# Optimization experiments

Measured on AMD Instinct MI355X. Metric: run time of the kernel, lower is better.

## Reference

```python
import jax, jax.numpy as jnp
import numpy as np

N_NODES = 500_000
N_EDGES = 2_000_000
N_GRAPHS = 20_000
N_PAIRS = 50_000
IN_CH = 64
EMB_CH = 64
HID_CH = 256
OUT_CH = 1


def setup_inputs() -> dict:
    key = jax.random.key(0)
    ks = jax.random.split(key, 10)
    x = jax.random.normal(ks[0], (N_NODES, IN_CH), dtype=jnp.float32)
    edge_index = jax.random.randint(ks[1], (2, N_EDGES), 0, N_NODES, dtype=jnp.int64)
    batch_idx = jnp.sort(jax.random.randint(ks[2], (N_NODES,), 0, N_GRAPHS, dtype=jnp.int64))
    drug_pairs = jax.random.randint(ks[3], (2, N_PAIRS), 0, N_GRAPHS, dtype=jnp.int64)
    s1 = 1.0 / np.sqrt(IN_CH)
    s2 = 1.0 / np.sqrt(EMB_CH)
    s3 = 1.0 / np.sqrt(2 * EMB_CH)
    s4 = 1.0 / np.sqrt(HID_CH)
    return {
        "x": x,
        "edge_index": edge_index,
        "batch_idx": batch_idx,
        "drug_pairs": drug_pairs,
        "W1": jax.random.normal(ks[4], (IN_CH, EMB_CH), jnp.float32) * s1,
        "b1": jnp.zeros((EMB_CH,), jnp.float32),
        "W2": jax.random.normal(ks[5], (EMB_CH, EMB_CH), jnp.float32) * s2,
        "b2": jnp.zeros((EMB_CH,), jnp.float32),
        "Wr1": jax.random.normal(ks[6], (2 * EMB_CH, HID_CH), jnp.float32) * s3,
        "br1": jnp.zeros((HID_CH,), jnp.float32),
        "Wr2": jax.random.normal(ks[7], (HID_CH, OUT_CH), jnp.float32) * s4,
        "br2": jnp.zeros((OUT_CH,), jnp.float32),
    }


def _gcn_conv(x, W, b, src, dst, num_nodes):
    # Standard GCNConv: x' = D^{-1/2} (A + I) D^{-1/2} (x W) + b,
    # with D the degree including self-loops.
    h = x @ W  # [N, C_out]
    ones = jnp.ones((src.shape[0],), h.dtype)
    deg = jax.ops.segment_sum(ones, dst, num_segments=num_nodes) + 1.0  # self-loop
    inv_sqrt = jax.lax.rsqrt(deg)
    norm = inv_sqrt[src] * inv_sqrt[dst]  # [E]
    msg = h[src] * norm[:, None]  # gather + scale, [E, C_out]
    agg = jax.ops.segment_sum(msg, dst, num_segments=num_nodes)
    agg = agg + h * (1.0 / deg)[:, None]  # self-loop term (norm = deg^{-1})
    return agg + b


def reference(x, edge_index, batch_idx, drug_pairs, W1, b1, W2, b2, Wr1, br1, Wr2, br2):
    n = x.shape[0]
    src, dst = edge_index[0], edge_index[1]
    # conv1 -> relu -> dropout(eval: identity)
    h = jax.nn.relu(_gcn_conv(x, W1, b1, src, dst, n))
    # conv2 -> relu -> dropout(eval: identity)
    h = jax.nn.relu(_gcn_conv(h, W2, b2, src, dst, n))
    # scatter_mean pooling: node embeds -> per-graph mean
    sums = jax.ops.segment_sum(h, batch_idx, num_segments=N_GRAPHS)
    counts = jax.ops.segment_sum(jnp.ones((n,), h.dtype), batch_idx, num_segments=N_GRAPHS)
    graph_embeds = sums / jnp.maximum(counts, 1.0)[:, None]  # [G, C]
    # gather drug pair embeddings and concat
    pair_feat = jnp.concatenate(
        [graph_embeds[drug_pairs[0]], graph_embeds[drug_pairs[1]]], axis=-1
    )  # [P, 2C]
    hid = jax.nn.relu(pair_feat @ Wr1 + br1)
    return hid @ Wr2 + br2  # [P, out_channels]
```

## Files before the change

### kernel.cpp

```cpp
#include <hip/hip_runtime.h>
#include <cstdint>

#define N_GRAPHS 20000
#define SCAN_CHUNK 2048
#define NBLK 512
#define SRC_BITS 19

typedef _Float16 half_t;
typedef __attribute__((ext_vector_type(4))) _Float16 half4;
typedef __attribute__((ext_vector_type(8))) _Float16 half8;
typedef __attribute__((ext_vector_type(4))) float f32x4;

__global__ __launch_bounds__(256) void scan1(const int* __restrict__ in, int* __restrict__ out,
                                             int* __restrict__ bsum, int M) {
  __shared__ int lds[256];
  int t = threadIdx.x;
  int base = blockIdx.x * SCAN_CHUNK + t * 8;
  int v[8];
  int s = 0;
#pragma unroll
  for (int i = 0; i < 8; ++i) {
    v[i] = (base + i < M) ? in[base + i] : 0;
    s += v[i];
  }
  lds[t] = s;
  __syncthreads();
  for (int off = 1; off < 256; off <<= 1) {
    int x = (t >= off) ? lds[t - off] : 0;
    __syncthreads();
    lds[t] += x;
    __syncthreads();
  }
  if (t == 255) bsum[blockIdx.x] = lds[255];
  int run = (t > 0) ? lds[t - 1] : 0;
#pragma unroll
  for (int i = 0; i < 8; ++i) {
    if (base + i <= M) out[base + i] = run;
    run += v[i];
  }
}

__global__ __launch_bounds__(256) void scan2(int* __restrict__ bsum, int nb) {
  __shared__ int lds[256];
  int t = threadIdx.x;
  lds[t] = (t < nb) ? bsum[t] : 0;
  __syncthreads();
  for (int off = 1; off < 256; off <<= 1) {
    int x = (t >= off) ? lds[t - off] : 0;
    __syncthreads();
    lds[t] += x;
    __syncthreads();
  }
  if (t < nb) bsum[t] = (t > 0) ? lds[t - 1] : 0;
}

__global__ void scan3(int* __restrict__ out, const int* __restrict__ bsum, int Mp1) {
  int i = blockIdx.x * blockDim.x + threadIdx.x;
  if (i < Mp1) out[i] += bsum[i / SCAN_CHUNK];
}

__global__ __launch_bounds__(256) void bucket_hist(const int* __restrict__ dst,
                                                   int* __restrict__ bcnt, int E, int nbuck) {
  __shared__ int h[512];
  for (int i = threadIdx.x; i < 512; i += 256) h[i] = 0;
  __syncthreads();
  int per = (E + NBLK - 1) / NBLK;
  int s = blockIdx.x * per;
  int e = min(s + per, E);
  for (int i = s + threadIdx.x; i < e; i += 256) atomicAdd(&h[dst[i] >> 10], 1);
  __syncthreads();
  for (int b = threadIdx.x; b < nbuck; b += 256) bcnt[(long)b * NBLK + blockIdx.x] = h[b];
}

__global__ __launch_bounds__(256) void bucket_scatter(const int* __restrict__ src,
                                                      const int* __restrict__ dst,
                                                      const int* __restrict__ bbase,
                                                      int* __restrict__ sed, int E, int nbuck) {
  __shared__ int h[512];
  for (int b = threadIdx.x; b < nbuck; b += 256) h[b] = bbase[(long)b * NBLK + blockIdx.x];
  __syncthreads();
  int per = (E + NBLK - 1) / NBLK;
  int s = blockIdx.x * per;
  int e = min(s + per, E);
  for (int i = s + threadIdx.x; i < e; i += 256) {
    int d = dst[i];
    int pos = atomicAdd(&h[d >> 10], 1);
    sed[pos] = ((d & 1023) << SRC_BITS) | src[i];
  }
}

__global__ __launch_bounds__(256) void node_csr(const int* __restrict__ sed,
                                                const int* __restrict__ bbase,
                                                int2* __restrict__ rsp, float* __restrict__ isq,
                                                int* __restrict__ csr, int E, int nbuck, int N,
                                                int PARK) {
  __shared__ int h[1024];
  __shared__ int ws[256];
  __shared__ int cur[1024];
  int b = blockIdx.x;
  int n0 = b << 10;
  int nn = min(1024, N - n0);
  int t = threadIdx.x;
  for (int i = t; i < 1024; i += 256) h[i] = 0;
  __syncthreads();
  int s = bbase[(long)b * NBLK];
  int e = (b + 1 < nbuck) ? bbase[(long)(b + 1) * NBLK] : E;
  for (int i = s + t; i < e; i += 256) atomicAdd(&h[((unsigned)sed[i]) >> SRC_BITS], 1);
  __syncthreads();
  int v0 = h[4 * t], v1 = h[4 * t + 1], v2 = h[4 * t + 2], v3 = h[4 * t + 3];
  int p0 = (v0 + 3) & ~3, p1 = (v1 + 3) & ~3, p2 = (v2 + 3) & ~3, p3 = (v3 + 3) & ~3;
  ws[t] = p0 + p1 + p2 + p3;
  __syncthreads();
  for (int off = 1; off < 256; off <<= 1) {
    int x = (t >= off) ? ws[t - off] : 0;
    __syncthreads();
    ws[t] += x;
    __syncthreads();
  }
  int pbase = s + 3072 * b;
  int st0 = pbase + ((t > 0) ? ws[t - 1] : 0);
  int st1 = st0 + p0, st2 = st1 + p1, st3 = st2 + p2;
  int i0 = 4 * t;
  cur[i0] = st0;
  cur[i0 + 1] = st1;
  cur[i0 + 2] = st2;
  cur[i0 + 3] = st3;
  if (i0 < nn) { rsp[n0 + i0] = make_int2(st0, st0 + p0); isq[n0 + i0] = rsqrtf((float)(v0 + 1)); }
  if (i0 + 1 < nn) { rsp[n0 + i0 + 1] = make_int2(st1, st1 + p1); isq[n0 + i0 + 1] = rsqrtf((float)(v1 + 1)); }
  if (i0 + 2 < nn) { rsp[n0 + i0 + 2] = make_int2(st2, st2 + p2); isq[n0 + i0 + 2] = rsqrtf((float)(v2 + 1)); }
  if (i0 + 3 < nn) { rsp[n0 + i0 + 3] = make_int2(st3, st3 + p3); isq[n0 + i0 + 3] = rsqrtf((float)(v3 + 1)); }
  __syncthreads();
  for (int i = s + t; i < e; i += 256) {
    int v = sed[i];
    int pos = atomicAdd(&cur[((unsigned)v) >> SRC_BITS], 1);
    csr[pos] = v & ((1 << SRC_BITS) - 1);
  }
  __syncthreads();
  for (int j = v0; j < p0; ++j) csr[st0 + j] = N;
  for (int j = v1; j < p1; ++j) csr[st1 + j] = N;
  for (int j = v2; j < p2; ++j) csr[st2 + j] = N;
  for (int j = v3; j < p3; ++j) csr[st3 + j] = N;
  if (b == 0 && t < 64) csr[PARK + t] = N;
}

__global__ __launch_bounds__(256) void scale_cast(const float* __restrict__ x,
                                                  const float* __restrict__ isq,
                                                  half_t* __restrict__ xs1,
                                                  half_t* __restrict__ xs2,
                                                  long nocts, int N) {
  long i = (long)blockIdx.x * 256 + threadIdx.x;
  if (blockIdx.x == 0 && threadIdx.x < 16) {
    const half8 z = {(half_t)0, (half_t)0, (half_t)0, (half_t)0,
                     (half_t)0, (half_t)0, (half_t)0, (half_t)0};
    half_t* base = (threadIdx.x < 8) ? xs1 : xs2;
    ((half8*)(base + (size_t)N * 64))[threadIdx.x & 7] = z;
  }
  if (i >= nocts) return;
  int node = (int)(i >> 3);
  float s = isq[node];
  float4 vlo = ((const float4*)x)[i * 2];
  float4 vhi = ((const float4*)x)[i * 2 + 1];
  half8 h;
  h[0] = (half_t)(vlo.x * s);
  h[1] = (half_t)(vlo.y * s);
  h[2] = (half_t)(vlo.z * s);
  h[3] = (half_t)(vlo.w * s);
  h[4] = (half_t)(vhi.x * s);
  h[5] = (half_t)(vhi.y * s);
  h[6] = (half_t)(vhi.z * s);
  h[7] = (half_t)(vhi.w * s);
  ((half8*)xs1)[i] = h;
}

__global__ __launch_bounds__(256) void gather_fused(const half_t* __restrict__ xs,
                                                    const int* __restrict__ csr,
                                                    const int2* __restrict__ rsp,
                                                    const float* __restrict__ isq,
                                                    const float* __restrict__ W,
                                                    const float* __restrict__ bias,
                                                    half_t* __restrict__ out, int N,
                                                    int PARK, int scale_out) {
  __shared__ half_t Wt[64][72];
  __shared__ half_t exh[32][72];
  __shared__ float idv[32];
  int tid = threadIdx.x;
  {
    int c = tid & 63;
    int kb = (tid >> 6) * 16;
#pragma unroll
    for (int i = 0; i < 16; ++i) Wt[c][kb + i] = (half_t)W[(kb + i) * 64 + c];
  }

  int lane = tid & 63;
  int sub = lane & 7;
  int grp = lane >> 3;
  int li = tid >> 3;
  int wid = (blockIdx.x * blockDim.x + tid) >> 6;
  long d0 = (long)wid * 8;
  int d = (int)d0 + grp;
  bool vd = (d0 < N) && (d < N);
  int dd = vd ? d : N - 1;
  int2 rr = rsp[dd];
  int jj = vd ? rr.x : PARK;
  int je = vd ? rr.y : PARK;
  float id = isq[dd];
  const uint8_t* xb = (const uint8_t*)xs;
  uint32_t co = (uint32_t)sub << 4;
  float ac[8];
  {
    half8 sv = *(const half8*)(xb + (((uint32_t)dd << 7) + co));
#pragma unroll
    for (int c = 0; c < 8; ++c) ac[c] = (float)sv[c];
  }
  jj = (jj < je) ? jj : PARK;
  while (__any(jj != PARK)) {
    int s0 = csr[jj];
    int s1 = csr[jj + 1];
    int s2 = csr[jj + 2];
    int s3 = csr[jj + 3];
    half8 v0 = *(const half8*)(xb + (((uint32_t)s0 << 7) + co));
    half8 v1 = *(const half8*)(xb + (((uint32_t)s1 << 7) + co));
    half8 v2 = *(const half8*)(xb + (((uint32_t)s2 << 7) + co));
    half8 v3 = *(const half8*)(xb + (((uint32_t)s3 << 7) + co));
    half8 sum = (v0 + v1) + (v2 + v3);
#pragma unroll
    for (int c = 0; c < 8; ++c) ac[c] += (float)sum[c];
    jj += 4;
    jj = (jj < je) ? jj : PARK;
  }
  {
    half8 ah;
#pragma unroll
    for (int c = 0; c < 8; ++c) ah[c] = (half_t)ac[c];
    *(half8*)&exh[li][sub * 8] = ah;
    if (sub == 0) idv[li] = id;
  }
  __syncthreads();

  int w = tid >> 6;
  int lr = lane & 15;
  int lk = lane >> 4;
  long d0b = (long)blockIdx.x * 32;
#pragma unroll
  for (int t2 = 0; t2 < 2; ++t2) {
    int tile = w * 2 + t2;
    int mt = tile >> 2;
    int nt = tile & 3;
    f32x4 acc = {0.f, 0.f, 0.f, 0.f};
#pragma unroll
    for (int ks = 0; ks < 2; ++ks) {
      half8 a = *(const half8*)&exh[mt * 16 + lr][ks * 32 + lk * 8];
      half8 b = *(const half8*)&Wt[nt * 16 + lr][ks * 32 + lk * 8];
      acc = __builtin_amdgcn_mfma_f32_16x16x32_f16(a, b, acc, 0, 0, 0);
    }
    float bv = bias[nt * 16 + lr];
#pragma unroll
    for (int j = 0; j < 4; ++j) {
      int nl = mt * 16 + lk * 4 + j;
      long dn = d0b + nl;
      if (dn < N) {
        float id2 = idv[nl];
        float m = scale_out ? id2 : 1.f;
        float r = fmaxf(fmaf(acc[j], id2, bv), 0.f) * m;
        out[dn * 64 + nt * 16 + lr] = (half_t)r;
      }
    }
  }
}

__global__ void seg_offsets(const int* __restrict__ batch, int* __restrict__ off, int N, int G) {
  int i = blockIdx.x * blockDim.x + threadIdx.x;
  if (i >= N) return;
  int b = batch[i];
  if (i == 0) {
    for (int g = 0; g <= b; ++g) off[g] = 0;
  } else {
    int pb = batch[i - 1];
    for (int g = pb + 1; g <= b; ++g) off[g] = i;
  }
  if (i == N - 1) {
    for (int g = b + 1; g <= G; ++g) off[g] = N;
  }
}

__global__ void pool_mean(const half_t* __restrict__ e2, const int* __restrict__ off,
                          float* __restrict__ ge, int G) {
  int lane = threadIdx.x & 63;
  int wid = (blockIdx.x * blockDim.x + threadIdx.x) >> 6;
  int nw = (gridDim.x * blockDim.x) >> 6;
  int c8 = lane & 7;
  int rp = lane >> 3;
  for (int g = wid; g < G; g += nw) {
    int s = off[g];
    int e = off[g + 1];
    float acc[8];
#pragma unroll
    for (int c = 0; c < 8; ++c) acc[c] = 0.f;
    for (int n = s + rp; n < e; n += 8) {
      half8 v = *(const half8*)&e2[(long)n * 64 + c8 * 8];
#pragma unroll
      for (int c = 0; c < 8; ++c) acc[c] += (float)v[c];
    }
#pragma unroll
    for (int c = 0; c < 8; ++c) {
      acc[c] += __shfl_xor(acc[c], 8, 64);
      acc[c] += __shfl_xor(acc[c], 16, 64);
      acc[c] += __shfl_xor(acc[c], 32, 64);
    }
    if (rp == 0) {
      float inv = 1.f / fmaxf((float)(e - s), 1.f);
      float4 lo = make_float4(acc[0] * inv, acc[1] * inv, acc[2] * inv, acc[3] * inv);
      float4 hi = make_float4(acc[4] * inv, acc[5] * inv, acc[6] * inv, acc[7] * inv);
      *(float4*)&ge[(long)g * 64 + c8 * 8] = lo;
      *(float4*)&ge[(long)g * 64 + c8 * 8 + 4] = hi;
    }
  }
}

#define PPB 64
__global__ __launch_bounds__(256) void pair_mlp(const float* __restrict__ ge,
                                                const int* __restrict__ dp,
                                                const float* __restrict__ Wr1,
                                                const float* __restrict__ br1,
                                                const float* __restrict__ Wr2,
                                                const float* __restrict__ br2,
                                                float* __restrict__ out, int P) {
  __shared__ float feat[PPB][128];
  __shared__ int pidx[2][PPB];
  int tid = threadIdx.x;
  int base = blockIdx.x * PPB;
  if (tid < PPB) {
    int p = base + tid;
    pidx[0][tid] = (p < P) ? dp[p] : 0;
    pidx[1][tid] = (p < P) ? dp[P + p] : 0;
  }
  __syncthreads();
#pragma unroll
  for (int i = 0; i < 8; ++i) {
    int u = tid + i * 256;
    int p = u >> 5;
    int k = (u & 31) * 4;
    int g = (k < 64) ? pidx[0][p] : pidx[1][p];
    *(float4*)&feat[p][k] = *(const float4*)&ge[(long)g * 64 + (k & 63)];
  }
  __syncthreads();
  int jg = tid & 63;
  int j0 = jg * 4;
  int pg = tid >> 6;
  int pb = pg * 16;
  float acc[16][4];
#pragma unroll
  for (int p = 0; p < 16; ++p)
#pragma unroll
    for (int j = 0; j < 4; ++j) acc[p][j] = 0.f;
  for (int k4 = 0; k4 < 32; ++k4) {
    float4 w0 = *(const float4*)&Wr1[(k4 * 4 + 0) * 256 + j0];
    float4 w1 = *(const float4*)&Wr1[(k4 * 4 + 1) * 256 + j0];
    float4 w2 = *(const float4*)&Wr1[(k4 * 4 + 2) * 256 + j0];
    float4 w3 = *(const float4*)&Wr1[(k4 * 4 + 3) * 256 + j0];
#pragma unroll
    for (int p = 0; p < 16; ++p) {
      float4 f = *(const float4*)&feat[pb + p][k4 * 4];
      acc[p][0] = fmaf(f.x, w0.x, acc[p][0]);
      acc[p][1] = fmaf(f.x, w0.y, acc[p][1]);
      acc[p][2] = fmaf(f.x, w0.z, acc[p][2]);
      acc[p][3] = fmaf(f.x, w0.w, acc[p][3]);
      acc[p][0] = fmaf(f.y, w1.x, acc[p][0]);
      acc[p][1] = fmaf(f.y, w1.y, acc[p][1]);
      acc[p][2] = fmaf(f.y, w1.z, acc[p][2]);
      acc[p][3] = fmaf(f.y, w1.w, acc[p][3]);
      acc[p][0] = fmaf(f.z, w2.x, acc[p][0]);
      acc[p][1] = fmaf(f.z, w2.y, acc[p][1]);
      acc[p][2] = fmaf(f.z, w2.z, acc[p][2]);
      acc[p][3] = fmaf(f.z, w2.w, acc[p][3]);
      acc[p][0] = fmaf(f.w, w3.x, acc[p][0]);
      acc[p][1] = fmaf(f.w, w3.y, acc[p][1]);
      acc[p][2] = fmaf(f.w, w3.z, acc[p][2]);
      acc[p][3] = fmaf(f.w, w3.w, acc[p][3]);
    }
  }
  float4 b1v = *(const float4*)&br1[j0];
  float4 w2v = *(const float4*)&Wr2[j0];
  float br2v = br2[0];
#pragma unroll
  for (int p = 0; p < 16; ++p) {
    float v = fmaxf(acc[p][0] + b1v.x, 0.f) * w2v.x;
    v = fmaf(fmaxf(acc[p][1] + b1v.y, 0.f), w2v.y, v);
    v = fmaf(fmaxf(acc[p][2] + b1v.z, 0.f), w2v.z, v);
    v = fmaf(fmaxf(acc[p][3] + b1v.w, 0.f), w2v.w, v);
    for (int o = 32; o > 0; o >>= 1) v += __shfl_down(v, o, 64);
    if (jg == 0) {
      int pp = base + pb + p;
      if (pp < P) out[pp] = v + br2v;
    }
  }
}

extern "C" void kernel_launch(void* const* d_in, const int* in_sizes, int n_in,
                              void* d_out, int out_size, void* d_ws, size_t ws_size,
                              hipStream_t stream) {
  const float* x = (const float*)d_in[0];
  const int* ei = (const int*)d_in[1];
  const int* batch = (const int*)d_in[2];
  const int* dp = (const int*)d_in[3];
  const float* W1 = (const float*)d_in[4];
  const float* b1 = (const float*)d_in[5];
  const float* W2 = (const float*)d_in[6];
  const float* b2 = (const float*)d_in[7];
  const float* Wr1 = (const float*)d_in[8];
  const float* br1 = (const float*)d_in[9];
  const float* Wr2 = (const float*)d_in[10];
  const float* br2 = (const float*)d_in[11];
  float* out = (float*)d_out;

  int N = in_sizes[0] / 64;
  int E = in_sizes[1] / 2;
  int P = in_sizes[3] / 2;
  int G = N_GRAPHS;
  const int* src = ei;
  const int* dstp = ei + E;

  int nbuck = (N + 1023) >> 10;
  long M = (long)nbuck * NBLK;
  int PARK = E + 3072 * nbuck;

  char* ws = (char*)d_ws;
  size_t o = 0;
  auto alloc = [&](size_t bytes) {
    void* p = ws + o;
    o += (bytes + 255) & ~(size_t)255;
    return p;
  };
  float* isq = (float*)alloc((size_t)N * 4);
  int2* rsp = (int2*)alloc((size_t)N * 8);
  int* bsum = (int*)alloc(1024 * 4);
  int* goff = (int*)alloc((size_t)(G + 1) * 4);
  int* bcnt = (int*)alloc((size_t)(M + 1) * 4);
  int* sed = (int*)alloc((size_t)E * 4);
  int* csr = (int*)alloc((size_t)(PARK + 80) * 4);
  half_t* xs1 = (half_t*)alloc((size_t)(N + 1) * 64 * 2);
  half_t* xs2 = (half_t*)alloc((size_t)(N + 1) * 64 * 2);
  half_t* abuf = (half_t*)alloc((size_t)N * 64 * 2);
  float* ge = (float*)alloc((size_t)G * 64 * 4);

  bucket_hist<<<NBLK, 256, 0, stream>>>(dstp, bcnt, E, nbuck);
  int nbA = (int)((M + SCAN_CHUNK - 1) / SCAN_CHUNK);
  scan1<<<nbA, 256, 0, stream>>>(bcnt, bcnt, bsum, (int)M);
  scan2<<<1, 256, 0, stream>>>(bsum, nbA);
  scan3<<<(int)((M + 1 + 255) / 256), 256, 0, stream>>>(bcnt, bsum, (int)(M + 1));
  bucket_scatter<<<NBLK, 256, 0, stream>>>(src, dstp, bcnt, sed, E, nbuck);
  node_csr<<<nbuck, 256, 0, stream>>>(sed, bcnt, rsp, isq, csr, E, nbuck, N, PARK);
  seg_offsets<<<(N + 255) / 256, 256, 0, stream>>>(batch, goff, N, G);

  long nocts = (long)N * 8;
  int gblocks = (N + 31) / 32;
  scale_cast<<<(int)((nocts + 255) / 256), 256, 0, stream>>>(x, isq, xs1, xs2, nocts, N);
  gather_fused<<<gblocks, 256, 0, stream>>>(xs1, csr, rsp, isq, W1, b1, xs2, N, PARK, 1);
  gather_fused<<<gblocks, 256, 0, stream>>>(xs2, csr, rsp, isq, W2, b2, abuf, N, PARK, 0);
  pool_mean<<<2048, 256, 0, stream>>>(abuf, goff, ge, G);
  pair_mlp<<<(P + PPB - 1) / PPB, 256, 0, stream>>>(ge, dp, Wr1, br1, Wr2, br2, out, P);
}
```

Before: 309.9 us.

## Compute pair MLP with fp16 MFMA and larger pair tiles

The pair regressor's first layer now runs on MFMA 16x16x32 fp16 instructions instead of scalar FMAs. Each block stages a transposed fp16 copy of Wr1 and 256 pair feature rows in padded LDS. The ReLU and second-layer dot product are fused into the MFMA epilogue with a shuffle reduction. This cuts the ALU cost of the MLP, but adds per-block weight conversion and fp16 rounding of the inputs.

```diff
diff --git a/kernel.cpp b/kernel.cpp
--- a/kernel.cpp
+++ b/kernel.cpp
@@ -317,7 +317,7 @@
   }
 }
 
-#define PPB 64
+#define PPB 256
 __global__ __launch_bounds__(256) void pair_mlp(const float* __restrict__ ge,
                                                 const int* __restrict__ dp,
                                                 const float* __restrict__ Wr1,
@@ -325,73 +325,81 @@
                                                 const float* __restrict__ Wr2,
                                                 const float* __restrict__ br2,
                                                 float* __restrict__ out, int P) {
-  __shared__ float feat[PPB][128];
-  __shared__ int pidx[2][PPB];
+  __shared__ half_t Wt[256][136];
+  __shared__ half_t ft[PPB][136];
   int tid = threadIdx.x;
+  for (int idx = tid; idx < 128 * 256; idx += 256) {
+    int k = idx >> 8;
+    int j = idx & 255;
+    Wt[j][k] = (half_t)Wr1[idx];
+  }
   int base = blockIdx.x * PPB;
-  if (tid < PPB) {
-    int p = base + tid;
-    pidx[0][tid] = (p < P) ? dp[p] : 0;
-    pidx[1][tid] = (p < P) ? dp[P + p] : 0;
-  }
-  __syncthreads();
-#pragma unroll
-  for (int i = 0; i < 8; ++i) {
-    int u = tid + i * 256;
-    int p = u >> 5;
-    int k = (u & 31) * 4;
-    int g = (k < 64) ? pidx[0][p] : pidx[1][p];
-    *(float4*)&feat[p][k] = *(const float4*)&ge[(long)g * 64 + (k & 63)];
-  }
-  __syncthreads();
-  int jg = tid & 63;
-  int j0 = jg * 4;
-  int pg = tid >> 6;
-  int pb = pg * 16;
-  float acc[16][4];
-#pragma unroll
-  for (int p = 0; p < 16; ++p)
-#pragma unroll
-    for (int j = 0; j < 4; ++j) acc[p][j] = 0.f;
-  for (int k4 = 0; k4 < 32; ++k4) {
-    float4 w0 = *(const float4*)&Wr1[(k4 * 4 + 0) * 256 + j0];
-    float4 w1 = *(const float4*)&Wr1[(k4 * 4 + 1) * 256 + j0];
-    float4 w2 = *(const float4*)&Wr1[(k4 * 4 + 2) * 256 + j0];
-    float4 w3 = *(const float4*)&Wr1[(k4 * 4 + 3) * 256 + j0];
-#pragma unroll
-    for (int p = 0; p < 16; ++p) {
-      float4 f = *(const float4*)&feat[pb + p][k4 * 4];
-      acc[p][0] = fmaf(f.x, w0.x, acc[p][0]);
-      acc[p][1] = fmaf(f.x, w0.y, acc[p][1]);
-      acc[p][2] = fmaf(f.x, w0.z, acc[p][2]);
-      acc[p][3] = fmaf(f.x, w0.w, acc[p][3]);
-      acc[p][0] = fmaf(f.y, w1.x, acc[p][0]);
-      acc[p][1] = fmaf(f.y, w1.y, acc[p][1]);
-      acc[p][2] = fmaf(f.y, w1.z, acc[p][2]);
-      acc[p][3] = fmaf(f.y, w1.w, acc[p][3]);
-      acc[p][0] = fmaf(f.z, w2.x, acc[p][0]);
-      acc[p][1] = fmaf(f.z, w2.y, acc[p][1]);
-      acc[p][2] = fmaf(f.z, w2.z, acc[p][2]);
-      acc[p][3] = fmaf(f.z, w2.w, acc[p][3]);
-      acc[p][0] = fmaf(f.w, w3.x, acc[p][0]);
-      acc[p][1] = fmaf(f.w, w3.y, acc[p][1]);
-      acc[p][2] = fmaf(f.w, w3.z, acc[p][2]);
-      acc[p][3] = fmaf(f.w, w3.w, acc[p][3]);
-    }
-  }
-  float4 b1v = *(const float4*)&br1[j0];
-  float4 w2v = *(const float4*)&Wr2[j0];
+  {
+    int pp = base + tid;
+    bool v = pp < P;
+    int ga = v ? dp[pp] : 0;
+    int gb = v ? dp[P + pp] : 0;
+#pragma unroll
+    for (int h = 0; h < 8; ++h) {
+      const float* srow = (h < 4) ? &ge[(long)ga * 64 + h * 16] : &ge[(long)gb * 64 + (h - 4) * 16];
+      float4 a0 = *(const float4*)&srow[0];
+      float4 a1 = *(const float4*)&srow[4];
+      float4 a2 = *(const float4*)&srow[8];
+      float4 a3 = *(const float4*)&srow[12];
+      half8 h0, h1;
+      h0[0] = (half_t)a0.x; h0[1] = (half_t)a0.y; h0[2] = (half_t)a0.z; h0[3] = (half_t)a0.w;
+      h0[4] = (half_t)a1.x; h0[5] = (half_t)a1.y; h0[6] = (half_t)a1.z; h0[7] = (half_t)a1.w;
+      h1[0] = (half_t)a2.x; h1[1] = (half_t)a2.y; h1[2] = (half_t)a2.z; h1[3] = (half_t)a2.w;
+      h1[4] = (half_t)a3.x; h1[5] = (half_t)a3.y; h1[6] = (half_t)a3.z; h1[7] = (half_t)a3.w;
+      *(half8*)&ft[tid][h * 16] = h0;
+      *(half8*)&ft[tid][h * 16 + 8] = h1;
+    }
+  }
+  __syncthreads();
+
+  int w = tid >> 6;
+  int lane = tid & 63;
+  int lr = lane & 15;
+  int lk = lane >> 4;
+  float b1v[16], w2v[16];
+#pragma unroll
+  for (int nt = 0; nt < 16; ++nt) {
+    b1v[nt] = br1[nt * 16 + lr];
+    w2v[nt] = Wr2[nt * 16 + lr];
+  }
   float br2v = br2[0];
 #pragma unroll
-  for (int p = 0; p < 16; ++p) {
-    float v = fmaxf(acc[p][0] + b1v.x, 0.f) * w2v.x;
-    v = fmaf(fmaxf(acc[p][1] + b1v.y, 0.f), w2v.y, v);
-    v = fmaf(fmaxf(acc[p][2] + b1v.z, 0.f), w2v.z, v);
-    v = fmaf(fmaxf(acc[p][3] + b1v.w, 0.f), w2v.w, v);
-    for (int o = 32; o > 0; o >>= 1) v += __shfl_down(v, o, 64);
-    if (jg == 0) {
-      int pp = base + pb + p;
-      if (pp < P) out[pp] = v + br2v;
+  for (int m4 = 0; m4 < 4; ++m4) {
+    int mt = w * 4 + m4;
+    float ps0 = 0.f, ps1 = 0.f, ps2 = 0.f, ps3 = 0.f;
+#pragma unroll
+    for (int nt = 0; nt < 16; ++nt) {
+      f32x4 acc = {0.f, 0.f, 0.f, 0.f};
+#pragma unroll
+      for (int ks = 0; ks < 4; ++ks) {
+        half8 a = *(const half8*)&ft[mt * 16 + lr][ks * 32 + lk * 8];
+        half8 b = *(const half8*)&Wt[nt * 16 + lr][ks * 32 + lk * 8];
+        acc = __builtin_amdgcn_mfma_f32_16x16x32_f16(a, b, acc, 0, 0, 0);
+      }
+      ps0 += fmaxf(acc[0] + b1v[nt], 0.f) * w2v[nt];
+      ps1 += fmaxf(acc[1] + b1v[nt], 0.f) * w2v[nt];
+      ps2 += fmaxf(acc[2] + b1v[nt], 0.f) * w2v[nt];
+      ps3 += fmaxf(acc[3] + b1v[nt], 0.f) * w2v[nt];
+    }
+#pragma unroll
+    for (int o = 1; o < 16; o <<= 1) {
+      ps0 += __shfl_xor(ps0, o, 64);
+      ps1 += __shfl_xor(ps1, o, 64);
+      ps2 += __shfl_xor(ps2, o, 64);
+      ps3 += __shfl_xor(ps3, o, 64);
+    }
+    if (lr == 0) {
+      int prow = mt * 16 + lk * 4;
+      int pp = base + prow;
+      if (pp + 0 < P) out[pp + 0] = ps0 + br2v;
+      if (pp + 1 < P) out[pp + 1] = ps1 + br2v;
+      if (pp + 2 < P) out[pp + 2] = ps2 + br2v;
+      if (pp + 3 < P) out[pp + 3] = ps3 + br2v;
     }
   }
 }
```

Measured after the change: 275.3 us (median of 2 runs). 1.13x faster.
